# Performance work log

Hardware: AMD Instinct MI355X
Metric: run time of the kernel (lower is better)

Reference implementation:

```python
import jax, jax.numpy as jnp
import numpy as np

NUM_HEADS = 32
HEAD_DIM = 128
NUM_KV_HEADS = 8
Q_LEN = 1024
MAX_SEQ = 4096
CACHE_BATCH = 4
SEQ_POS = 1024
BATCH_POS = 1


def setup_inputs() -> dict:
    key = jax.random.key(0)
    ks = jax.random.split(key, 6)
    query_state = jax.random.normal(ks[0], (1, NUM_HEADS, Q_LEN, HEAD_DIM), jnp.float32)
    key_state = jax.random.normal(ks[1], (1, NUM_KV_HEADS, Q_LEN, HEAD_DIM), jnp.float32)
    value_state = jax.random.normal(ks[2], (1, NUM_KV_HEADS, Q_LEN, HEAD_DIM), jnp.float32)
    past_key_state = jax.random.normal(ks[3], (CACHE_BATCH, NUM_KV_HEADS, MAX_SEQ, HEAD_DIM), jnp.float32)
    past_value_state = jax.random.normal(ks[4], (CACHE_BATCH, NUM_KV_HEADS, MAX_SEQ, HEAD_DIM), jnp.float32)
    # Causal prefill mask: query token i (global pos SEQ_POS+i) may attend to cache pos m <= SEQ_POS+i
    i = jnp.arange(Q_LEN)[:, None] + SEQ_POS
    j = jnp.arange(MAX_SEQ)[None, :]
    attn_mask = (j <= i).astype(jnp.float32)[None, None]  # [1,1,Q_LEN,MAX_SEQ]
    scale = jnp.array([1.0 / np.sqrt(HEAD_DIM)], jnp.float32)
    return {
        "query_state": query_state,
        "key_state": key_state,
        "value_state": value_state,
        "attn_mask": attn_mask,
        "batch_position": BATCH_POS,
        "past_key_state": past_key_state,
        "past_value_state": past_value_state,
        "seq_position": SEQ_POS,
        "scale": scale,
    }


def reference(query_state, key_state, value_state, attn_mask, batch_position,
              past_key_state, past_value_state, seq_position, scale):
    g = NUM_HEADS // NUM_KV_HEADS
    q_len = query_state.shape[2]
    # --- cache update (prefill: insert new K/V at [batch_position, :, seq_position:seq_position+q_len]) ---
    k_cache = jax.lax.dynamic_update_slice(past_key_state, key_state, (batch_position, 0, seq_position, 0))
    v_cache = jax.lax.dynamic_update_slice(past_value_state, value_state, (batch_position, 0, seq_position, 0))
    # --- grouped-query attention over the updated cache row ---
    q = query_state.reshape(1, NUM_KV_HEADS, g, q_len, HEAD_DIM)
    k = jax.lax.dynamic_slice_in_dim(k_cache, batch_position, 1, axis=0)[0]  # [kvh, MAX_SEQ, hd]
    v = jax.lax.dynamic_slice_in_dim(v_cache, batch_position, 1, axis=0)[0]
    scores = jnp.einsum('bkgqd,kmd->bkgqm', q, k) * scale[0]  # [1,kvh,g,q,MAX_SEQ]
    neg = jnp.finfo(scores.dtype).min
    scores = jnp.where(attn_mask[:, :, None] > 0.5, scores, neg)
    probs = jax.nn.softmax(scores, axis=-1)
    out = jnp.einsum('bkgqm,kmd->bkgqd', probs, v)  # [1,kvh,g,q,hd]
    out = out.reshape(1, NUM_HEADS, q_len, HEAD_DIM)
    attn_output = out.transpose(0, 2, 1, 3).reshape(1, q_len, NUM_HEADS * HEAD_DIM)
    return attn_output, k_cache, v_cache
```

## Files before the change

kernel.cpp:

```cpp
#include <hip/hip_runtime.h>

#define NH 32
#define KVHN 8
#define HD 128
#define QL 1024
#define MS 4096
#define KVB 64

typedef __bf16 bf16x8 __attribute__((ext_vector_type(8)));
typedef __bf16 bf16x4 __attribute__((ext_vector_type(4)));
typedef float f32x4 __attribute__((ext_vector_type(4)));
typedef float f32x16 __attribute__((ext_vector_type(16)));
typedef unsigned int u32x4 __attribute__((ext_vector_type(4)));


__device__ __forceinline__ void gload16(const void* g, void* l) {
    __builtin_amdgcn_global_load_lds(
        (const __attribute__((address_space(1))) unsigned int*)g,
        (__attribute__((address_space(3))) unsigned int*)l, 16, 0, 0);
}

__device__ __forceinline__ unsigned int pk2(float a, float b) {
    union { __bf16 h; unsigned short u; } x, y;
    x.h = (__bf16)a; y.h = (__bf16)b;
    return (unsigned int)x.u | ((unsigned int)y.u << 16);
}

__device__ __forceinline__ float exp2fast(float x) {
    return __builtin_amdgcn_exp2f(x);
}

__device__ __forceinline__ u32x4 nt_load(const u32x4* p) {
    return __builtin_nontemporal_load(p);
}
__device__ __forceinline__ void nt_store(u32x4* p, u32x4 v) {
    __builtin_nontemporal_store(v, p);
}

__global__ __launch_bounds__(256) void pack_kernel(
    const float4* __restrict__ kn, const float4* __restrict__ vn,
    const float4* __restrict__ pk, const float4* __restrict__ pv,
    const int* __restrict__ bp_p, const int* __restrict__ sp_p,
    __bf16* __restrict__ kbf, __bf16* __restrict__ vt)
{
    __shared__ float vtile[8][132];
    int li = blockIdx.x * 256 + threadIdx.x;
    int bp = *bp_p, sp = *sp_p;
    int d4  = li & 31;
    int pos = (li >> 5) & 4095;
    int kvh = li >> 17;
    float4 kv4, vv4;
    if (pos >= sp && pos < sp + QL) {
        int ns = (kvh * QL + (pos - sp)) * 32 + d4;
        kv4 = kn[ns]; vv4 = vn[ns];
    } else {
        int gi = (bp << 20) + li;
        kv4 = pk[gi]; vv4 = pv[gi];
    }
    {
        bf16x4 o;
        o[0] = (__bf16)kv4.x; o[1] = (__bf16)kv4.y;
        o[2] = (__bf16)kv4.z; o[3] = (__bf16)kv4.w;
        int c16 = d4 >> 1, half = d4 & 1;
        *(bf16x4*)(kbf + ((size_t)kvh * MS + pos) * HD
                       + ((c16 ^ (pos & 7)) * 8 + half * 4)) = o;
        *(float4*)&vtile[threadIdx.x >> 5][d4 * 4] = vv4;
    }
    __syncthreads();
    if (threadIdx.x < 128) {
        int d  = threadIdx.x;
        int p0 = (blockIdx.x * 8) & 4095;
        int pt = p0 >> 6, chk = (p0 & 63) >> 3;
        bf16x8 o;
        #pragma unroll
        for (int j = 0; j < 8; ++j) o[j] = (__bf16)vtile[j][d];
        *(bf16x8*)(vt + (((size_t)kvh * 64 + pt) * HD + d) * 64
                      + ((chk ^ (d & 7)) * 8)) = o;
    }
}

__global__ __launch_bounds__(256, 2) void mega_kernel(
    const float* __restrict__ q,
    const int* __restrict__ bp_p, const int* __restrict__ sp_p,
    const float* __restrict__ scale_p,
    const __bf16* __restrict__ kbf, const __bf16* __restrict__ vt,
    const float4* __restrict__ knf, const float4* __restrict__ vnf,
    const float4* __restrict__ pkf, const float4* __restrict__ pvf,
    float4* __restrict__ okf, float4* __restrict__ ovf,
    float* __restrict__ out)
{
    __shared__ __align__(16) unsigned char smem[32768];

    const int bid = blockIdx.x;
    const int tid = threadIdx.x;
    const int sp  = *sp_p;
    const int bp  = *bp_p;

    if ((bid >> 8) & 1) {
        int cslot = (bid < 512) ? (bid - 256) : (bid - 768) + 256;
        const u32x4* csrc_new  = (const u32x4*)((cslot < 256) ? knf : vnf);
        const u32x4* csrc_past = (const u32x4*)((cslot < 256) ? pkf : pvf);
        u32x4*       cdst      = (u32x4*)((cslot < 256) ? okf : ovf);
        const int    cbase     = (cslot & 255) * 16384;
        for (int s = 0; s < 16; ++s) {
            u32x4 t[4];
            #pragma unroll
            for (int jj = 0; jj < 4; ++jj) {
                int idx = cbase + s * 1024 + jj * 256 + tid;
                int d4  = idx & 31;
                int pos = (idx >> 5) & 4095;
                int ck  = (idx >> 17) & 7;
                int b   = idx >> 20;
                t[jj] = (b == bp && pos >= sp && pos < sp + QL)
                    ? nt_load(&csrc_new[(ck * QL + (pos - sp)) * 32 + d4])
                    : nt_load(&csrc_past[idx]);
            }
            #pragma unroll
            for (int jj = 0; jj < 4; ++jj)
                nt_store(&cdst[cbase + s * 1024 + jj * 256 + tid], t[jj]);
        }
        return;
    }

    const int attnIdx = (bid < 256) ? bid : bid - 256;
    const float scl = *scale_p * 1.44269504088896340736f;

    int kvh = attnIdx & 7;
    int inner = (attnIdx & 255) >> 3;
    int headLocal = inner & 3;
    int j = inner >> 2;
    int qtile = (attnIdx < 256) ? j : 15 - j;
    int head = kvh * 4 + headLocal;

    const int q0     = qtile * 64;
    const int wave   = tid >> 6;
    const int qsub   = wave & 1;
    const int kvhalf = wave >> 1;
    const int lane   = tid & 63;
    const int hi     = lane >> 5;
    const int c31    = lane & 31;
    const int qb     = q0 + qsub * 32;
    const int myq    = qb + c31;

    const unsigned char* krow = (const unsigned char*)(kbf + (size_t)kvh * MS * HD);
    const unsigned char* vrow = (const unsigned char*)(vt + (size_t)kvh * 64 * HD * 64);

    bf16x8 qf[8];
    #pragma unroll
    for (int dc = 0; dc < 8; ++dc) {
        const float* src = q + ((size_t)(head * QL + qb + c31) * HD + dc * 16 + hi * 8);
        float4 f0 = *(const float4*)src;
        float4 f1 = *(const float4*)(src + 4);
        bf16x8 v;
        v[0]=(__bf16)(f0.x*scl); v[1]=(__bf16)(f0.y*scl);
        v[2]=(__bf16)(f0.z*scl); v[3]=(__bf16)(f0.w*scl);
        v[4]=(__bf16)(f1.x*scl); v[5]=(__bf16)(f1.y*scl);
        v[6]=(__bf16)(f1.z*scl); v[7]=(__bf16)(f1.w*scl);
        qf[dc] = v;
    }

    f32x16 acc[4];
    #pragma unroll
    for (int dsub = 0; dsub < 4; ++dsub)
        #pragma unroll
        for (int r = 0; r < 16; ++r) acc[dsub][r] = 0.f;
    float m_run = -1e30f, l_run = 0.f;

    const int n_super = (sp + q0 + 64) >> 6;

    auto stageK = [&](int buf, int t) {
        const unsigned char* kt = krow + (size_t)t * 16384;
        unsigned char* kl = smem + buf * 16384;
        #pragma unroll
        for (int p = 0; p < 4; ++p) {
            int off = p * 4096 + tid * 16;
            gload16(kt + off, kl + off);
        }
    };

    int cur = 0;
    stageK(0, 0);
    __syncthreads();

    for (int it = 0; it < n_super; ++it) {
        const int n0 = it * KVB + kvhalf * 32;

        u32x4 vraw[4][2];
        {
            const unsigned char* vtb = vrow + (size_t)it * 16384;
            #pragma unroll
            for (int dsub = 0; dsub < 4; ++dsub) {
                #pragma unroll
                for (int qd = 0; qd < 2; ++qd) {
                    int vr = dsub * 32 + c31;
                    int ksg = kvhalf * 2 + qd;
                    vraw[dsub][qd] = *(const u32x4*)(vtb + vr * 128
                        + (((ksg * 2 + hi) ^ (vr & 7)) << 4));
                }
            }
        }
        __builtin_amdgcn_sched_barrier(0);
        if (it + 1 < n_super) stageK(cur ^ 1, it + 1);

        const unsigned char* Ksm = smem + cur * 16384;

        f32x16 st0, st1;
        #pragma unroll
        for (int r = 0; r < 16; ++r) { st0[r] = 0.f; st1[r] = 0.f; }
        int kr = kvhalf * 32 + c31;
        __builtin_amdgcn_s_setprio(1);
        #pragma unroll
        for (int dc = 0; dc < 4; ++dc) {
            bf16x8 ka = *(const bf16x8*)(Ksm + kr * 256 + (((2 * dc + hi) ^ (kr & 7)) << 4));
            st0 = __builtin_amdgcn_mfma_f32_32x32x16_bf16(ka, qf[dc], st0, 0, 0, 0);
            bf16x8 kb = *(const bf16x8*)(Ksm + kr * 256 + (((2 * (dc + 4) + hi) ^ (kr & 7)) << 4));
            st1 = __builtin_amdgcn_mfma_f32_32x32x16_bf16(kb, qf[dc + 4], st1, 0, 0, 0);
        }
        __builtin_amdgcn_s_setprio(0);
        f32x16 st = st0 + st1;

        const bool need_mask = (n0 + 31) > (sp + qb);
        if (need_mask) {
            #pragma unroll
            for (int r = 0; r < 16; ++r) {
                int kvg = n0 + (r & 3) + 8 * (r >> 2) + 4 * hi;
                if (kvg > sp + myq) st[r] = -1e30f;
            }
        }
        float m01 = fmaxf(fmaxf(st[0], st[1]), fmaxf(st[2], st[3]));
        float m23 = fmaxf(fmaxf(st[4], st[5]), fmaxf(st[6], st[7]));
        float m45 = fmaxf(fmaxf(st[8], st[9]), fmaxf(st[10], st[11]));
        float m67 = fmaxf(fmaxf(st[12], st[13]), fmaxf(st[14], st[15]));
        float mx = fmaxf(fmaxf(m01, m23), fmaxf(m45, m67));
        mx = fmaxf(mx, __shfl_xor(mx, 32));

        if (!__all(mx <= m_run + 8.0f)) {
            float nm = fmaxf(m_run, mx);
            float corr = exp2fast(m_run - nm);
            m_run = nm;
            l_run *= corr;
            #pragma unroll
            for (int r = 0; r < 16; ++r) {
                int qsrc = (r & 3) + 8 * (r >> 2) + 4 * hi;
                float cq = __shfl(corr, qsrc);
                acc[0][r] *= cq; acc[1][r] *= cq; acc[2][r] *= cq; acc[3][r] *= cq;
            }
        }

        #pragma unroll
        for (int r = 0; r < 16; ++r) st[r] = exp2fast(st[r] - m_run);
        {
            float s0 = (st[0] + st[1]) + (st[2] + st[3]);
            float s1 = (st[4] + st[5]) + (st[6] + st[7]);
            float s2 = (st[8] + st[9]) + (st[10] + st[11]);
            float s3 = (st[12] + st[13]) + (st[14] + st[15]);
            l_run += (s0 + s1) + (s2 + s3);
        }

        unsigned int loW[4], hiW[4];
        #pragma unroll
        for (int qd = 0; qd < 2; ++qd) {
            int b = qd * 8;
            loW[qd*2+0] = pk2(st[b+0], st[b+1]);
            loW[qd*2+1] = pk2(st[b+2], st[b+3]);
            hiW[qd*2+0] = pk2(st[b+4], st[b+5]);
            hiW[qd*2+1] = pk2(st[b+6], st[b+7]);
        }
        bf16x8 pfrag[2];
        #pragma unroll
        for (int qd = 0; qd < 2; ++qd) {
            unsigned int a0 = loW[qd*2+0], b0 = hiW[qd*2+0];
            unsigned int a1 = loW[qd*2+1], b1 = hiW[qd*2+1];
            asm("v_permlane32_swap_b32 %0, %1" : "+v"(a0), "+v"(b0));
            asm("v_permlane32_swap_b32 %0, %1" : "+v"(a1), "+v"(b1));
            union { unsigned int u[4]; bf16x8 v; } fu;
            fu.u[0] = a0; fu.u[1] = a1; fu.u[2] = b0; fu.u[3] = b1;
            pfrag[qd] = fu.v;
        }

        __builtin_amdgcn_s_setprio(1);
        #pragma unroll
        for (int dsub = 0; dsub < 4; ++dsub) {
            #pragma unroll
            for (int qd = 0; qd < 2; ++qd) {
                union { u32x4 u; bf16x8 v; } cvt;
                cvt.u = vraw[dsub][qd];
                acc[dsub] = __builtin_amdgcn_mfma_f32_32x32x16_bf16(pfrag[qd], cvt.v, acc[dsub], 0, 0, 0);
            }
        }
        __builtin_amdgcn_s_setprio(0);

        __syncthreads();
        cur ^= 1;
    }

    float l_full = l_run + __shfl_xor(l_run, 32);
    float* mlm = (float*)smem;
    float* mll = (float*)smem + 128;
    if (hi == 0) { mlm[wave * 32 + c31] = m_run; mll[wave * 32 + c31] = l_full; }
    __syncthreads();
    int pw = wave ^ 2;
    float m_o = mlm[pw * 32 + c31];
    float l_o = mll[pw * 32 + c31];
    float m_n = fmaxf(m_run, m_o);
    float sc   = exp2fast(m_run - m_n);
    float sc_o = exp2fast(m_o - m_n);
    float linv = 1.0f / (l_full * sc + l_o * sc_o);
    __bf16* Oex = (__bf16*)(smem + 1024) + (size_t)qsub * 32 * 128;
    if (kvhalf) {
        #pragma unroll
        for (int r = 0; r < 16; ++r) {
            int qsrc = (r & 3) + 8 * (r >> 2) + 4 * hi;
            float s = __shfl(sc, qsrc);
            #pragma unroll
            for (int dsub = 0; dsub < 4; ++dsub)
                Oex[qsrc * 128 + dsub * 32 + c31] = (__bf16)(acc[dsub][r] * s);
        }
    }
    __syncthreads();
    if (!kvhalf) {
        #pragma unroll
        for (int r = 0; r < 16; ++r) {
            int qsrc = (r & 3) + 8 * (r >> 2) + 4 * hi;
            float s  = __shfl(sc, qsrc);
            float lq = __shfl(linv, qsrc);
            float* orow = out + (size_t)(qb + qsrc) * (NH * HD) + head * HD;
            #pragma unroll
            for (int dsub = 0; dsub < 4; ++dsub)
                orow[dsub * 32 + c31] =
                    (acc[dsub][r] * s + (float)Oex[qsrc * 128 + dsub * 32 + c31]) * lq;
        }
    }
}

extern "C" void kernel_launch(void* const* d_in, const int* in_sizes, int n_in,
                              void* d_out, int out_size, void* d_ws, size_t ws_size,
                              hipStream_t stream)
{
    const float* q_st   = (const float*)d_in[0];
    const float* k_new  = (const float*)d_in[1];
    const float* v_new  = (const float*)d_in[2];
    const int*   bp_p   = (const int*)d_in[4];
    const float* past_k = (const float*)d_in[5];
    const float* past_v = (const float*)d_in[6];
    const int*   sp_p   = (const int*)d_in[7];
    const float* scl_p  = (const float*)d_in[8];

    float* out_attn = (float*)d_out;
    float* out_k    = out_attn + (size_t)QL * NH * HD;
    float* out_v    = out_k + (size_t)4 * KVHN * MS * HD;

    __bf16* kbf = (__bf16*)d_ws;
    __bf16* vtw = kbf + (size_t)KVHN * MS * HD;

    pack_kernel<<<4096, 256, 0, stream>>>(
        (const float4*)k_new, (const float4*)v_new,
        (const float4*)past_k, (const float4*)past_v,
        bp_p, sp_p, kbf, vtw);

    mega_kernel<<<1024, 256, 0, stream>>>(
        q_st, bp_p, sp_p, scl_p, kbf, vtw,
        (const float4*)k_new, (const float4*)v_new,
        (const float4*)past_k, (const float4*)past_v,
        (float4*)out_k, (float4*)out_v, out_attn);
}
```

Measured before the change: 103.4 us.

## Load K tiles directly into registers with double-buffered prefetch instead of LDS

Replaces the LDS-staged K tile pipeline (global_load_lds into double-buffered shared memory plus a per-iteration __syncthreads) with direct global-to-register loads of each wave's K fragments. The loop is unrolled by two and alternates two register buffers so the next tile's K loads overlap the current tile's compute. This removes the block-wide barrier and cuts shared memory from 32 KB to 17 KB, but raises register pressure (16 extra u32x4 per thread) under launch_bounds(256,2). It also makes waves fetch K redundantly from global/L2 rather than sharing one LDS copy.

```diff
diff --git a/kernel.cpp b/kernel.cpp
--- a/kernel.cpp
+++ b/kernel.cpp
@@ -13,12 +13,6 @@
 typedef float f32x16 __attribute__((ext_vector_type(16)));
 typedef unsigned int u32x4 __attribute__((ext_vector_type(4)));
 
-
-__device__ __forceinline__ void gload16(const void* g, void* l) {
-    __builtin_amdgcn_global_load_lds(
-        (const __attribute__((address_space(1))) unsigned int*)g,
-        (__attribute__((address_space(3))) unsigned int*)l, 16, 0, 0);
-}
 
 __device__ __forceinline__ unsigned int pk2(float a, float b) {
     union { __bf16 h; unsigned short u; } x, y;
@@ -89,7 +83,7 @@
     float4* __restrict__ okf, float4* __restrict__ ovf,
     float* __restrict__ out)
 {
-    __shared__ __align__(16) unsigned char smem[32768];
+    __shared__ __align__(16) unsigned char smem[17408];
 
     const int bid = blockIdx.x;
     const int tid = threadIdx.x;
@@ -167,54 +161,40 @@
     float m_run = -1e30f, l_run = 0.f;
 
     const int n_super = (sp + q0 + 64) >> 6;
-
-    auto stageK = [&](int buf, int t) {
-        const unsigned char* kt = krow + (size_t)t * 16384;
-        unsigned char* kl = smem + buf * 16384;
-        #pragma unroll
-        for (int p = 0; p < 4; ++p) {
-            int off = p * 4096 + tid * 16;
-            gload16(kt + off, kl + off);
-        }
+    const int kr = kvhalf * 32 + c31;
+
+    auto loadK = [&](int t, u32x4* kd) {
+        const unsigned char* ktb = krow + (size_t)t * 16384;
+        #pragma unroll
+        for (int dc = 0; dc < 8; ++dc)
+            kd[dc] = *(const u32x4*)(ktb + kr * 256 + (((2 * dc + hi) ^ (kr & 7)) << 4));
     };
 
-    int cur = 0;
-    stageK(0, 0);
-    __syncthreads();
-
-    for (int it = 0; it < n_super; ++it) {
+    auto compute = [&](int it, const u32x4* kd) {
         const int n0 = it * KVB + kvhalf * 32;
 
         u32x4 vraw[4][2];
-        {
-            const unsigned char* vtb = vrow + (size_t)it * 16384;
-            #pragma unroll
-            for (int dsub = 0; dsub < 4; ++dsub) {
-                #pragma unroll
-                for (int qd = 0; qd < 2; ++qd) {
-                    int vr = dsub * 32 + c31;
-                    int ksg = kvhalf * 2 + qd;
-                    vraw[dsub][qd] = *(const u32x4*)(vtb + vr * 128
-                        + (((ksg * 2 + hi) ^ (vr & 7)) << 4));
-                }
-            }
-        }
-        __builtin_amdgcn_sched_barrier(0);
-        if (it + 1 < n_super) stageK(cur ^ 1, it + 1);
-
-        const unsigned char* Ksm = smem + cur * 16384;
+        const unsigned char* vtb = vrow + (size_t)it * 16384;
+        #pragma unroll
+        for (int dsub = 0; dsub < 4; ++dsub)
+            #pragma unroll
+            for (int qd = 0; qd < 2; ++qd) {
+                int vr = dsub * 32 + c31;
+                int ksg = kvhalf * 2 + qd;
+                vraw[dsub][qd] = *(const u32x4*)(vtb + vr * 128
+                    + (((ksg * 2 + hi) ^ (vr & 7)) << 4));
+            }
 
         f32x16 st0, st1;
         #pragma unroll
         for (int r = 0; r < 16; ++r) { st0[r] = 0.f; st1[r] = 0.f; }
-        int kr = kvhalf * 32 + c31;
         __builtin_amdgcn_s_setprio(1);
         #pragma unroll
         for (int dc = 0; dc < 4; ++dc) {
-            bf16x8 ka = *(const bf16x8*)(Ksm + kr * 256 + (((2 * dc + hi) ^ (kr & 7)) << 4));
-            st0 = __builtin_amdgcn_mfma_f32_32x32x16_bf16(ka, qf[dc], st0, 0, 0, 0);
-            bf16x8 kb = *(const bf16x8*)(Ksm + kr * 256 + (((2 * (dc + 4) + hi) ^ (kr & 7)) << 4));
-            st1 = __builtin_amdgcn_mfma_f32_32x32x16_bf16(kb, qf[dc + 4], st1, 0, 0, 0);
+            union { u32x4 u; bf16x8 v; } ca, cb;
+            ca.u = kd[dc]; cb.u = kd[dc + 4];
+            st0 = __builtin_amdgcn_mfma_f32_32x32x16_bf16(ca.v, qf[dc], st0, 0, 0, 0);
+            st1 = __builtin_amdgcn_mfma_f32_32x32x16_bf16(cb.v, qf[dc + 4], st1, 0, 0, 0);
         }
         __builtin_amdgcn_s_setprio(0);
         f32x16 st = st0 + st1;
@@ -289,10 +269,18 @@
             }
         }
         __builtin_amdgcn_s_setprio(0);
-
-        __syncthreads();
-        cur ^= 1;
-    }
+    };
+
+    u32x4 kA[8], kB[8];
+    loadK(0, kA);
+    int t2 = 0;
+    for (; t2 + 1 < n_super; t2 += 2) {
+        loadK(t2 + 1, kB);
+        compute(t2, kA);
+        if (t2 + 2 < n_super) loadK(t2 + 2, kA);
+        compute(t2 + 1, kB);
+    }
+    if (t2 < n_super) compute(t2, kA);
 
     float l_full = l_run + __shfl_xor(l_run, 32);
     float* mlm = (float*)smem;
```

Measured after the change: 182.0 us. 76.0% more time.

## Shrink attention blocks to 32 queries with two waves and separate copy blocks

Applied to the files above, without the earlier changes.

Attention workgroups drop from four waves covering 64 queries to two waves covering 32 queries, doubling the attention block count to 1024 with a new zigzag q-tile ordering. Cache-copy blocks move to a contiguous tail range of 512 two-wave blocks, each issuing eight loads per step. The aim is finer causal load balancing and higher occupancy. The cost is that each K/V tile staged in shared memory now serves half as many queries, doubling K/V traffic per query, and the copy work is interleaved differently with attention.

```diff
diff --git a/kernel.cpp b/kernel.cpp
--- a/kernel.cpp
+++ b/kernel.cpp
@@ -79,7 +79,7 @@
     }
 }
 
-__global__ __launch_bounds__(256, 2) void mega_kernel(
+__global__ __launch_bounds__(128, 4) void mega_kernel(
     const float* __restrict__ q,
     const int* __restrict__ bp_p, const int* __restrict__ sp_p,
     const float* __restrict__ scale_p,
@@ -96,17 +96,17 @@
     const int sp  = *sp_p;
     const int bp  = *bp_p;
 
-    if ((bid >> 8) & 1) {
-        int cslot = (bid < 512) ? (bid - 256) : (bid - 768) + 256;
-        const u32x4* csrc_new  = (const u32x4*)((cslot < 256) ? knf : vnf);
-        const u32x4* csrc_past = (const u32x4*)((cslot < 256) ? pkf : pvf);
-        u32x4*       cdst      = (u32x4*)((cslot < 256) ? okf : ovf);
-        const int    cbase     = (cslot & 255) * 16384;
+    if (bid >= 1024) {
+        int cidx = bid - 1024;
+        const u32x4* csrc_new  = (const u32x4*)((cidx < 256) ? knf : vnf);
+        const u32x4* csrc_past = (const u32x4*)((cidx < 256) ? pkf : pvf);
+        u32x4*       cdst      = (u32x4*)((cidx < 256) ? okf : ovf);
+        const int    cbase     = (cidx & 255) * 16384;
         for (int s = 0; s < 16; ++s) {
-            u32x4 t[4];
-            #pragma unroll
-            for (int jj = 0; jj < 4; ++jj) {
-                int idx = cbase + s * 1024 + jj * 256 + tid;
+            u32x4 t[8];
+            #pragma unroll
+            for (int jj = 0; jj < 8; ++jj) {
+                int idx = cbase + s * 1024 + jj * 128 + tid;
                 int d4  = idx & 31;
                 int pos = (idx >> 5) & 4095;
                 int ck  = (idx >> 17) & 7;
@@ -116,30 +116,28 @@
                     : nt_load(&csrc_past[idx]);
             }
             #pragma unroll
-            for (int jj = 0; jj < 4; ++jj)
-                nt_store(&cdst[cbase + s * 1024 + jj * 256 + tid], t[jj]);
+            for (int jj = 0; jj < 8; ++jj)
+                nt_store(&cdst[cbase + s * 1024 + jj * 128 + tid], t[jj]);
         }
         return;
     }
 
-    const int attnIdx = (bid < 256) ? bid : bid - 256;
+    const int aidx = bid;
     const float scl = *scale_p * 1.44269504088896340736f;
 
-    int kvh = attnIdx & 7;
-    int inner = (attnIdx & 255) >> 3;
-    int headLocal = inner & 3;
-    int j = inner >> 2;
-    int qtile = (attnIdx < 256) ? j : 15 - j;
+    int kvh = aidx & 7;
+    int headLocal = (aidx >> 3) & 3;
+    int q5 = aidx >> 5;
+    int qtile = (q5 & 1) ? (31 - (q5 >> 1)) : (q5 >> 1);
     int head = kvh * 4 + headLocal;
 
-    const int q0     = qtile * 64;
+    const int q0     = qtile * 32;
     const int wave   = tid >> 6;
-    const int qsub   = wave & 1;
-    const int kvhalf = wave >> 1;
+    const int kvhalf = wave;
     const int lane   = tid & 63;
     const int hi     = lane >> 5;
     const int c31    = lane & 31;
-    const int qb     = q0 + qsub * 32;
+    const int qb     = q0;
     const int myq    = qb + c31;
 
     const unsigned char* krow = (const unsigned char*)(kbf + (size_t)kvh * MS * HD);
@@ -166,14 +164,14 @@
         for (int r = 0; r < 16; ++r) acc[dsub][r] = 0.f;
     float m_run = -1e30f, l_run = 0.f;
 
-    const int n_super = (sp + q0 + 64) >> 6;
+    const int n_super = (sp + q0 + 32 + 63) >> 6;
 
     auto stageK = [&](int buf, int t) {
         const unsigned char* kt = krow + (size_t)t * 16384;
         unsigned char* kl = smem + buf * 16384;
         #pragma unroll
-        for (int p = 0; p < 4; ++p) {
-            int off = p * 4096 + tid * 16;
+        for (int p = 0; p < 8; ++p) {
+            int off = p * 2048 + tid * 16;
             gload16(kt + off, kl + off);
         }
     };
@@ -296,17 +294,17 @@
 
     float l_full = l_run + __shfl_xor(l_run, 32);
     float* mlm = (float*)smem;
-    float* mll = (float*)smem + 128;
+    float* mll = (float*)smem + 64;
     if (hi == 0) { mlm[wave * 32 + c31] = m_run; mll[wave * 32 + c31] = l_full; }
     __syncthreads();
-    int pw = wave ^ 2;
+    int pw = wave ^ 1;
     float m_o = mlm[pw * 32 + c31];
     float l_o = mll[pw * 32 + c31];
     float m_n = fmaxf(m_run, m_o);
     float sc   = exp2fast(m_run - m_n);
     float sc_o = exp2fast(m_o - m_n);
     float linv = 1.0f / (l_full * sc + l_o * sc_o);
-    __bf16* Oex = (__bf16*)(smem + 1024) + (size_t)qsub * 32 * 128;
+    __bf16* Oex = (__bf16*)(smem + 1024);
     if (kvhalf) {
         #pragma unroll
         for (int r = 0; r < 16; ++r) {
@@ -358,7 +356,7 @@
         (const float4*)past_k, (const float4*)past_v,
         bp_p, sp_p, kbf, vtw);
 
-    mega_kernel<<<1024, 256, 0, stream>>>(
+    mega_kernel<<<1536, 128, 0, stream>>>(
         q_st, bp_p, sp_p, scl_p, kbf, vtw,
         (const float4*)k_new, (const float4*)v_new,
         (const float4*)past_k, (const float4*)past_v,
```

Result: slower. 133.6 us (+29.2%).
